# Kernel optimization log

Measured on AMD Instinct MI355X. Metric: run time of the kernel, lower is better.

Reference implementation:

```python
import jax, jax.numpy as jnp
import numpy as np
import math

NUM_HEADS = 8
FDIM = 64
NUM_BUCKETS = 32
MAX_DISTANCE = 128


def _relative_position_bucket(rel_pos, num_buckets=NUM_BUCKETS, max_distance=MAX_DISTANCE):
    nb = num_buckets // 2
    ret = (rel_pos >= 0).astype(jnp.int32) * nb
    n = jnp.abs(rel_pos)
    max_exact = nb // 2
    is_small = n < max_exact
    # safe log: clamp n to >=1 where large-branch is unused
    val_large = max_exact + (
        jnp.log(jnp.maximum(n, 1).astype(jnp.float32) / max_exact)
        / math.log(max_distance / max_exact) * (nb - max_exact)
    ).astype(jnp.int32)
    val_large = jnp.minimum(val_large, nb - 1)
    return ret + jnp.where(is_small, n, val_large)


def setup_inputs() -> dict:
    key = jax.random.key(0)
    k = jax.random.split(key, 5)
    B, Nin, F, T = 4, 64, FDIM, 1024
    N = NUM_HEADS * FDIM
    x = jax.random.normal(k[0], (B, Nin, F, T), dtype=jnp.float32)
    # kaiming_normal: std = 1/sqrt(fan_in)
    w_in = jax.random.normal(k[1], (NUM_HEADS, Nin), dtype=jnp.float32) / np.sqrt(Nin)
    w_qk = jax.random.normal(k[2], (2 * N, N), dtype=jnp.float32) / np.sqrt(N)
    w_out = jax.random.normal(k[3], (Nin, NUM_HEADS), dtype=jnp.float32) / np.sqrt(NUM_HEADS)
    rel_bias = jax.random.normal(k[4], (NUM_BUCKETS, NUM_HEADS), dtype=jnp.float32) * 0.02
    return {"x": x, "w_in": w_in, "w_qk": w_qk, "w_out": w_out, "rel_bias": rel_bias}


def reference(x, w_in, w_qk, w_out, rel_bias):
    B, Nin, F, T = x.shape
    h, f = NUM_HEADS, FDIM
    scale = f ** (-0.5)
    # proj_in: 1x1 conv2d Nin -> h
    xi = jnp.einsum('bcft,hc->bhft', x, w_in)          # [B,h,F,T]
    xr = xi.reshape(B, h * f, T)                        # b (h f) t
    v = xr.reshape(B, h, f, T).transpose(0, 1, 3, 2)    # [B,h,T,f]
    # qk: 1x1 conv1d N -> 2N
    qk = jnp.einsum('bct,dc->bdt', xr, w_qk)            # [B,2N,T]
    qk = qk.reshape(B, h, 2 * f, T).transpose(0, 1, 3, 2)  # [B,h,T,2f]
    q, k = qk[..., :f], qk[..., f:]
    sim = jnp.einsum('bhnd,bhmd->bhnm', q, k)           # [B,h,T,T]
    # relative position bias
    q_pos = jnp.arange(T)
    k_pos = jnp.arange(T)
    rel = k_pos[None, :] - q_pos[:, None]               # [T,T]
    buckets = _relative_position_bucket(rel)
    bias = rel_bias[buckets]                            # [T,T,h]
    bias = bias.transpose(2, 0, 1)[None]                # [1,h,T,T]
    sim = (sim + bias) * scale
    attn = jax.nn.softmax(sim, axis=-1)
    out = jnp.einsum('bhnm,bhmd->bhnd', attn, v)        # [B,h,T,f]
    out = out.transpose(0, 1, 3, 2)                     # [B,h,f,T]
    out = jnp.einsum('bhft,ch->bcft', out, w_out)       # [B,Nin,F,T]
    return out
```

## Files before the change

### kernel.cpp

```cpp
#include <hip/hip_runtime.h>
#include <math.h>

#define QSCALE 0.18033688011112042f

typedef __attribute__((ext_vector_type(4))) float  f32x4;
typedef __attribute__((ext_vector_type(2))) float  f32x2;
typedef __attribute__((ext_vector_type(8))) short  bf16x8;
typedef __attribute__((ext_vector_type(4))) short  bf16x4;
typedef __attribute__((ext_vector_type(4))) int    i32x4;

static __device__ __forceinline__ short f2bf(float f) {
    union { float f; unsigned u; } v; v.f = f;
    unsigned r = v.u + 0x7fffu + ((v.u >> 16) & 1u);
    return (short)(r >> 16);
}
static __device__ __forceinline__ int pk2bf(float a, float b) {
    return ((int)f2bf(a) & 0xffff) | ((int)f2bf(b) << 16);
}

#define MFMA16(A,B,C) __builtin_amdgcn_mfma_f32_16x16x32_bf16(A, B, C, 0, 0, 0)

__global__ void k_prep(const float* __restrict__ wqk, short* __restrict__ wqk_b) {
    int i = blockIdx.x * 256 + threadIdx.x;
    int D = i >> 9;
    float s = (D & 64) ? 1.0f : QSCALE;
    wqk_b[i] = f2bf(wqk[i] * s);
}

__global__ __launch_bounds__(256) void k_proj_in(
    const float* __restrict__ x, const float* __restrict__ w_in,
    short* __restrict__ xi_v, short* __restrict__ xr_t)
{
    __shared__ float w_s[512];
    __shared__ __align__(16) short tr[64 * 72];
    int tid = threadIdx.x;
    int tx = tid & 31, fy = tid >> 5;
    int tb = blockIdx.x, fb = blockIdx.y, b = blockIdx.z;
    w_s[tid] = w_in[tid & 511];
    w_s[(tid + 256) & 511] = w_in[(tid + 256) & 511];
    __syncthreads();

    int f = fb * 8 + fy;
    int t = tb * 64 + tx * 2;
    float acc[8][2];
    #pragma unroll
    for (int h = 0; h < 8; h++) { acc[h][0] = 0.f; acc[h][1] = 0.f; }

    const float* xp = x + ((size_t)b * 64 * 64 + (size_t)f) * 1024 + t;
    f32x2 buf[8];
    #pragma unroll
    for (int i = 0; i < 8; i++) buf[i] = *(const f32x2*)&xp[(size_t)i * 65536];
    #pragma unroll
    for (int c8 = 0; c8 < 64; c8 += 8) {
        f32x2 cur[8];
        #pragma unroll
        for (int i = 0; i < 8; i++) cur[i] = buf[i];
        if (c8 + 8 < 64) {
            #pragma unroll
            for (int i = 0; i < 8; i++)
                buf[i] = *(const f32x2*)&xp[(size_t)(c8 + 8 + i) * 65536];
        }
        #pragma unroll
        for (int i = 0; i < 8; i++)
            #pragma unroll
            for (int h = 0; h < 8; h++) {
                float wv = w_s[h * 64 + c8 + i];
                acc[h][0] = fmaf(cur[i][0], wv, acc[h][0]);
                acc[h][1] = fmaf(cur[i][1], wv, acc[h][1]);
            }
    }
    #pragma unroll
    for (int h = 0; h < 8; h++)
        *(int*)&xi_v[(((size_t)b * 8 + h) * 64 + f) * 1024 + t] = pk2bf(acc[h][0], acc[h][1]);
    #pragma unroll
    for (int h = 0; h < 8; h++) {
        tr[(tx * 2 + 0) * 72 + h * 8 + fy] = f2bf(acc[h][0]);
        tr[(tx * 2 + 1) * 72 + h * 8 + fy] = f2bf(acc[h][1]);
    }
    __syncthreads();
    int h2 = tid & 7, trow = tid >> 3;
    #pragma unroll
    for (int i = 0; i < 2; i++) {
        int t2 = trow + i * 32;
        i32x4 v = *(const i32x4*)&tr[t2 * 72 + h2 * 8];
        *(i32x4*)&xr_t[((size_t)b * 1024 + tb * 64 + t2) * 512 + h2 * 64 + fb * 8] = v;
    }
}

__global__ __launch_bounds__(256, 4) void k_qk(
    const short* __restrict__ wqk_b, const short* __restrict__ xr_t,
    short* __restrict__ qk_t)
{
    __shared__ __align__(16) short As[64 * 72];
    __shared__ __align__(16) short Bs[64 * 72];
    int tid = threadIdx.x;
    int w = tid >> 6, lane = tid & 63;
    int quad = lane >> 4, l16 = lane & 15;
    int t0 = blockIdx.x * 64;
    int Dt = blockIdx.y;
    int b  = blockIdx.z;

    f32x4 acc[4];
    #pragma unroll
    for (int tt = 0; tt < 4; tt++) acc[tt] = (f32x4){0.f,0.f,0.f,0.f};

    const short* Ag = wqk_b + (size_t)Dt * 64 * 512;
    const short* Bg = xr_t + ((size_t)b * 1024 + t0) * 512;

    int s_row = tid >> 2, s_col = (tid & 3) * 16;

    for (int kk = 0; kk < 512; kk += 64) {
        __syncthreads();
        #pragma unroll
        for (int i = 0; i < 2; i++) {
            *(i32x4*)&As[s_row * 72 + s_col + i * 8] =
                *(const i32x4*)&Ag[(size_t)s_row * 512 + kk + s_col + i * 8];
            *(i32x4*)&Bs[s_row * 72 + s_col + i * 8] =
                *(const i32x4*)&Bg[(size_t)s_row * 512 + kk + s_col + i * 8];
        }
        __syncthreads();
        bf16x8 af[2];
        #pragma unroll
        for (int kc = 0; kc < 2; kc++)
            af[kc] = *(const bf16x8*)&As[(w * 16 + l16) * 72 + kc * 32 + quad * 8];
        #pragma unroll
        for (int tt = 0; tt < 4; tt++) {
            bf16x8 bf0 = *(const bf16x8*)&Bs[(tt * 16 + l16) * 72 + quad * 8];
            bf16x8 bf1 = *(const bf16x8*)&Bs[(tt * 16 + l16) * 72 + 32 + quad * 8];
            acc[tt] = MFMA16(af[0], bf0, acc[tt]);
            acc[tt] = MFMA16(af[1], bf1, acc[tt]);
        }
    }
    int h = Dt >> 1;
    int d2 = (Dt & 1) * 64 + w * 16 + quad * 4;
    #pragma unroll
    for (int tt = 0; tt < 4; tt++) {
        bf16x4 pk;
        pk.x = f2bf(acc[tt][0]); pk.y = f2bf(acc[tt][1]);
        pk.z = f2bf(acc[tt][2]); pk.w = f2bf(acc[tt][3]);
        int t = t0 + tt * 16 + l16;
        *(bf16x4*)&qk_t[(((size_t)b * 8 + h) * 1024 + t) * 128 + d2] = pk;
    }
}

__global__ __launch_bounds__(256, 4) void k_attn(
    const short* __restrict__ qk_t, const short* __restrict__ xi_v,
    const float* __restrict__ rel_bias, float* __restrict__ o_part,
    float* __restrict__ lsum)
{
    __shared__ __align__(16) short Ks[64 * 72];
    __shared__ __align__(16) short Vs[64 * 72];
    __shared__ __align__(16) short Ps[4][16 * 72];
    __shared__ float elut[2048];
    int tid = threadIdx.x;
    int w = tid >> 6, lane = tid & 63;
    int quad = lane >> 4, l16 = lane & 15;
    int nb = blockIdx.x, bh = blockIdx.y, mh = blockIdx.z;
    int h = bh & 7;
    int n_base = nb * 64;

    for (int i = tid; i < 2047; i += 256) {
        int rel = i - 1023;
        int ret = (rel >= 0) ? 16 : 0;
        int na = rel < 0 ? -rel : rel;
        int idx;
        if (na < 8) idx = ret + na;
        else {
            int vl = 8 + (int)(log2f((float)na * 0.125f) * 2.0f);
            vl = vl > 15 ? 15 : vl;
            idx = ret + vl;
        }
        elut[i] = exp2f(rel_bias[idx * 8 + h] * QSCALE);
    }

    const short* qb = qk_t + (size_t)bh * (1024 * 128);
    const short* vb = xi_v + (size_t)bh * (64 * 1024);

    bf16x8 qf[2];
    #pragma unroll
    for (int kk = 0; kk < 2; kk++)
        qf[kk] = *(const bf16x8*)&qb[(size_t)(n_base + w * 16 + l16) * 128 + kk * 32 + quad * 8];

    f32x4 acc_o[4];
    #pragma unroll
    for (int dt = 0; dt < 4; dt++) acc_o[dt] = (f32x4){0.f,0.f,0.f,0.f};
    float l_st = 0.f;

    int srow = tid >> 2;
    int soff = (tid & 3) * 16;
    int m0 = mh * 512;
    i32x4 gk[2], gv[2];
    #pragma unroll
    for (int i = 0; i < 2; i++) {
        gk[i] = *(const i32x4*)&qb[(size_t)(m0 + srow) * 128 + 64 + soff + i * 8];
        gv[i] = *(const i32x4*)&vb[(size_t)srow * 1024 + m0 + soff + i * 8];
    }

    __syncthreads();

    #pragma unroll 1
    for (int it = 0; it < 8; it++) {
        *(i32x4*)&Ks[srow * 72 + soff]     = gk[0];
        *(i32x4*)&Ks[srow * 72 + soff + 8] = gk[1];
        *(i32x4*)&Vs[srow * 72 + soff]     = gv[0];
        *(i32x4*)&Vs[srow * 72 + soff + 8] = gv[1];
        __syncthreads();
        if (it < 7) {
            int m1 = m0 + 64;
            #pragma unroll
            for (int i = 0; i < 2; i++) {
                gk[i] = *(const i32x4*)&qb[(size_t)(m1 + srow) * 128 + 64 + soff + i * 8];
                gv[i] = *(const i32x4*)&vb[(size_t)srow * 1024 + m1 + soff + i * 8];
            }
        }

        f32x4 s[4];
        #pragma unroll
        for (int mt = 0; mt < 4; mt++) {
            bf16x8 kf0 = *(const bf16x8*)&Ks[(mt * 16 + l16) * 72 + quad * 8];
            bf16x8 kf1 = *(const bf16x8*)&Ks[(mt * 16 + l16) * 72 + 32 + quad * 8];
            f32x4 tacc = (f32x4){0.f,0.f,0.f,0.f};
            tacc = MFMA16(kf0, qf[0], tacc);
            tacc = MFMA16(kf1, qf[1], tacc);
            s[mt] = tacc;
        }

        int n = n_base + w * 16 + l16;
        #pragma unroll
        for (int mt = 0; mt < 4; mt++) {
            int rel0 = m0 + mt * 16 + quad * 4 - n + 1023;
            #pragma unroll
            for (int j = 0; j < 4; j++) {
                float p = exp2f(s[mt][j]) * elut[rel0 + j];
                s[mt][j] = p;
                l_st += p;
            }
        }
        #pragma unroll
        for (int mt = 0; mt < 4; mt++) {
            bf16x4 pk;
            pk.x = f2bf(s[mt][0]); pk.y = f2bf(s[mt][1]);
            pk.z = f2bf(s[mt][2]); pk.w = f2bf(s[mt][3]);
            *(bf16x4*)&Ps[w][l16 * 72 + mt * 16 + quad * 4] = pk;
        }
        #pragma unroll
        for (int si = 0; si < 2; si++) {
            bf16x8 pf = *(const bf16x8*)&Ps[w][l16 * 72 + si * 32 + quad * 8];
            #pragma unroll
            for (int dt = 0; dt < 4; dt++) {
                bf16x8 vf = *(const bf16x8*)&Vs[(dt * 16 + l16) * 72 + si * 32 + quad * 8];
                acc_o[dt] = MFMA16(pf, vf, acc_o[dt]);
            }
        }
        m0 += 64;
        __syncthreads();
    }
    #pragma unroll
    for (int dt = 0; dt < 4; dt++)
        *(f32x4*)&o_part[(((size_t)mh * 32 + bh) * 64 + dt * 16 + l16) * 1024 + n_base + w * 16 + quad * 4] = acc_o[dt];
    l_st += __shfl_xor(l_st, 16);
    l_st += __shfl_xor(l_st, 32);
    if (quad == 0)
        lsum[((size_t)bh * 2 + mh) * 1024 + n_base + w * 16 + l16] = l_st;
}

__global__ __launch_bounds__(512) void k_proj_out(
    const float* __restrict__ o_part, const float* __restrict__ lsum,
    const float* __restrict__ w_out, float* __restrict__ out)
{
    __shared__ float w_s[512];
    __shared__ float o_s[8][64];
    int tid = threadIdx.x;
    int tx = tid & 63, ty = tid >> 6;
    int tb = blockIdx.x, f = blockIdx.y, b = blockIdx.z;
    w_s[tid] = w_out[tid];
    int t = tb * 64 + tx;
    int bh = b * 8 + ty;
    float l0 = lsum[((size_t)bh * 2 + 0) * 1024 + t];
    float l1 = lsum[((size_t)bh * 2 + 1) * 1024 + t];
    float o0 = o_part[((size_t)(0 * 32 + bh) * 64 + f) * 1024 + t];
    float o1 = o_part[((size_t)(1 * 32 + bh) * 64 + f) * 1024 + t];
    o_s[ty][tx] = (o0 + o1) / (l0 + l1);
    __syncthreads();
    float ov[8];
    #pragma unroll
    for (int hh = 0; hh < 8; hh++) ov[hh] = o_s[hh][tx];
    #pragma unroll
    for (int j = 0; j < 8; j++) {
        int c = ty * 8 + j;
        float a = 0.f;
        #pragma unroll
        for (int hh = 0; hh < 8; hh++) a = fmaf(ov[hh], w_s[c * 8 + hh], a);
        out[(((size_t)b * 64 + c) * 64 + f) * 1024 + t] = a;
    }
}

extern "C" void kernel_launch(void* const* d_in, const int* in_sizes, int n_in,
                              void* d_out, int out_size, void* d_ws, size_t ws_size,
                              hipStream_t stream)
{
    const float* x        = (const float*)d_in[0];
    const float* w_in     = (const float*)d_in[1];
    const float* w_qk     = (const float*)d_in[2];
    const float* w_out    = (const float*)d_in[3];
    const float* rel_bias = (const float*)d_in[4];
    float* out = (float*)d_out;

    char* ws = (char*)d_ws;
    short* wqk_b  = (short*)(ws);
    short* xi_v   = (short*)(ws + (size_t)1  * (1 << 20));
    short* xr_t   = (short*)(ws + (size_t)5  * (1 << 20));
    short* qk_t   = (short*)(ws + (size_t)9  * (1 << 20));
    float* o_part = (float*)(ws + (size_t)17 * (1 << 20));
    float* lsum   = (float*)(ws + (size_t)33 * (1 << 20));

    hipLaunchKernelGGL(k_prep,     dim3(2048),       dim3(256), 0, stream, w_qk, wqk_b);
    hipLaunchKernelGGL(k_proj_in,  dim3(16, 8, 4),   dim3(256), 0, stream, x, w_in, xi_v, xr_t);
    hipLaunchKernelGGL(k_qk,       dim3(16, 16, 4),  dim3(256), 0, stream, wqk_b, xr_t, qk_t);
    hipLaunchKernelGGL(k_attn,     dim3(16, 32, 2),  dim3(256), 0, stream, qk_t, xi_v, rel_bias, o_part, lsum);
    hipLaunchKernelGGL(k_proj_out, dim3(16, 64, 4),  dim3(512), 0, stream, o_part, lsum, w_out, out);
}
```

Measured before the change: 163.5 us.

## Split attention key range across waves and reduce partial outputs in shared memory

The attention kernel now gives each wave a disjoint slice of keys for all 64 query rows, instead of a 16-row query slice over all keys. K and V fragments are loaded straight from global memory into registers, which removes the shared K/V staging and the per-iteration barriers. The bias LUT is shrunk to the 576 relative offsets this block actually touches and stored as rotated bf16 copies for aligned vector reads. Partial outputs from the four waves are summed through shared memory before one coalesced store. This trades more accumulator registers (occupancy hint lowered to 3), lower bias precision and a serialized cross-wave reduction for fewer LDS round-trips and syncs.

```diff
diff --git a/kernel.cpp b/kernel.cpp
--- a/kernel.cpp
+++ b/kernel.cpp
@@ -16,6 +16,10 @@
 }
 static __device__ __forceinline__ int pk2bf(float a, float b) {
     return ((int)f2bf(a) & 0xffff) | ((int)f2bf(b) << 16);
+}
+static __device__ __forceinline__ float bf2f(short s) {
+    union { unsigned u; float f; } v; v.u = ((unsigned)(unsigned short)s) << 16;
+    return v.f;
 }
 
 #define MFMA16(A,B,C) __builtin_amdgcn_mfma_f32_16x16x32_bf16(A, B, C, 0, 0, 0)
@@ -143,24 +147,26 @@
     }
 }
 
-__global__ __launch_bounds__(256, 4) void k_attn(
+__global__ __launch_bounds__(256, 3) void k_attn(
     const short* __restrict__ qk_t, const short* __restrict__ xi_v,
     const float* __restrict__ rel_bias, float* __restrict__ o_part,
     float* __restrict__ lsum)
 {
-    __shared__ __align__(16) short Ks[64 * 72];
-    __shared__ __align__(16) short Vs[64 * 72];
-    __shared__ __align__(16) short Ps[4][16 * 72];
-    __shared__ float elut[2048];
+    __shared__ __align__(16) short Ps[4][64 * 40];
+    __shared__ __align__(16) short lut_rot[4][144 * 4];
+    __shared__ __align__(16) float Or[64 * 68];
+    __shared__ float lsum_s[4][64];
+
     int tid = threadIdx.x;
     int w = tid >> 6, lane = tid & 63;
     int quad = lane >> 4, l16 = lane & 15;
     int nb = blockIdx.x, bh = blockIdx.y, mh = blockIdx.z;
     int h = bh & 7;
     int n_base = nb * 64;
-
-    for (int i = tid; i < 2047; i += 256) {
-        int rel = i - 1023;
+    int base_rel = mh * 512 - n_base - 63;
+
+    for (int i = tid; i < 576; i += 256) {
+        int rel = base_rel + i;
         int ret = (rel >= 0) ? 16 : 0;
         int na = rel < 0 ? -rel : rel;
         int idx;
@@ -170,98 +176,117 @@
             vl = vl > 15 ? 15 : vl;
             idx = ret + vl;
         }
-        elut[i] = exp2f(rel_bias[idx * 8 + h] * QSCALE);
-    }
+        Or[i] = exp2f(rel_bias[idx * 8 + h] * QSCALE);
+    }
+    __syncthreads();
+    for (int e = tid; e < 576; e += 256) {
+        int r = e / 144, k = e - r * 144;
+        int i0 = 4 * k + r;
+        bf16x4 pk;
+        pk.x = f2bf(Or[i0 > 575 ? 575 : i0]);
+        pk.y = f2bf(Or[i0 + 1 > 575 ? 575 : i0 + 1]);
+        pk.z = f2bf(Or[i0 + 2 > 575 ? 575 : i0 + 2]);
+        pk.w = f2bf(Or[i0 + 3 > 575 ? 575 : i0 + 3]);
+        *(bf16x4*)&lut_rot[r][k * 4] = pk;
+    }
+    __syncthreads();
 
     const short* qb = qk_t + (size_t)bh * (1024 * 128);
     const short* vb = xi_v + (size_t)bh * (64 * 1024);
 
-    bf16x8 qf[2];
-    #pragma unroll
-    for (int kk = 0; kk < 2; kk++)
-        qf[kk] = *(const bf16x8*)&qb[(size_t)(n_base + w * 16 + l16) * 128 + kk * 32 + quad * 8];
-
-    f32x4 acc_o[4];
-    #pragma unroll
-    for (int dt = 0; dt < 4; dt++) acc_o[dt] = (f32x4){0.f,0.f,0.f,0.f};
-    float l_st = 0.f;
-
-    int srow = tid >> 2;
-    int soff = (tid & 3) * 16;
-    int m0 = mh * 512;
-    i32x4 gk[2], gv[2];
-    #pragma unroll
-    for (int i = 0; i < 2; i++) {
-        gk[i] = *(const i32x4*)&qb[(size_t)(m0 + srow) * 128 + 64 + soff + i * 8];
-        gv[i] = *(const i32x4*)&vb[(size_t)srow * 1024 + m0 + soff + i * 8];
-    }
-
-    __syncthreads();
+    bf16x8 qf[4][2];
+    #pragma unroll
+    for (int nt = 0; nt < 4; nt++)
+        #pragma unroll
+        for (int kc = 0; kc < 2; kc++)
+            qf[nt][kc] = *(const bf16x8*)&qb[(size_t)(n_base + nt * 16 + l16) * 128 + kc * 32 + quad * 8];
+
+    f32x4 acc[4][4];
+    #pragma unroll
+    for (int nt = 0; nt < 4; nt++)
+        #pragma unroll
+        for (int dt = 0; dt < 4; dt++) acc[nt][dt] = (f32x4){0.f,0.f,0.f,0.f};
+    f32x4 lp = (f32x4){0.f,0.f,0.f,0.f};
+
+    short* psw = &Ps[w][0];
 
     #pragma unroll 1
-    for (int it = 0; it < 8; it++) {
-        *(i32x4*)&Ks[srow * 72 + soff]     = gk[0];
-        *(i32x4*)&Ks[srow * 72 + soff + 8] = gk[1];
-        *(i32x4*)&Vs[srow * 72 + soff]     = gv[0];
-        *(i32x4*)&Vs[srow * 72 + soff + 8] = gv[1];
+    for (int it = 0; it < 4; it++) {
+        int mloc  = it * 128 + w * 32;
+        int mbase = mh * 512 + mloc;
+        bf16x8 vf[4];
+        #pragma unroll
+        for (int dt = 0; dt < 4; dt++)
+            vf[dt] = *(const bf16x8*)&vb[(size_t)(dt * 16 + l16) * 1024 + mbase + quad * 8];
+
+        #pragma unroll
+        for (int mt = 0; mt < 2; mt++) {
+            bf16x8 kf0 = *(const bf16x8*)&qb[(size_t)(mbase + mt * 16 + l16) * 128 + 64 + quad * 8];
+            bf16x8 kf1 = *(const bf16x8*)&qb[(size_t)(mbase + mt * 16 + l16) * 128 + 96 + quad * 8];
+            #pragma unroll
+            for (int nt = 0; nt < 4; nt++) {
+                f32x4 s = (f32x4){0.f,0.f,0.f,0.f};
+                s = MFMA16(kf0, qf[nt][0], s);
+                s = MFMA16(kf1, qf[nt][1], s);
+                int rel0 = mloc + mt * 16 + quad * 4 - (nt * 16 + l16) + 63;
+                bf16x4 lv = *(const bf16x4*)&lut_rot[rel0 & 3][(rel0 >> 2) * 4];
+                f32x4 p;
+                p[0] = exp2f(s[0]) * bf2f(lv.x);
+                p[1] = exp2f(s[1]) * bf2f(lv.y);
+                p[2] = exp2f(s[2]) * bf2f(lv.z);
+                p[3] = exp2f(s[3]) * bf2f(lv.w);
+                lp[nt] += p[0] + p[1] + p[2] + p[3];
+                bf16x4 pk;
+                pk.x = f2bf(p[0]); pk.y = f2bf(p[1]);
+                pk.z = f2bf(p[2]); pk.w = f2bf(p[3]);
+                *(bf16x4*)&psw[(nt * 16 + l16) * 40 + mt * 16 + quad * 4] = pk;
+            }
+        }
+        #pragma unroll
+        for (int nt = 0; nt < 4; nt++) {
+            bf16x8 pf = *(const bf16x8*)&psw[(nt * 16 + l16) * 40 + quad * 8];
+            #pragma unroll
+            for (int dt = 0; dt < 4; dt++)
+                acc[nt][dt] = MFMA16(pf, vf[dt], acc[nt][dt]);
+        }
+    }
+
+    #pragma unroll
+    for (int nt = 0; nt < 4; nt++) {
+        float v = lp[nt];
+        v += __shfl_xor(v, 16);
+        v += __shfl_xor(v, 32);
+        if (quad == 0) lsum_s[w][nt * 16 + l16] = v;
+    }
+    __syncthreads();
+
+    #pragma unroll 1
+    for (int ww = 0; ww < 4; ww++) {
+        if (w == ww) {
+            #pragma unroll
+            for (int nt = 0; nt < 4; nt++)
+                #pragma unroll
+                for (int dt = 0; dt < 4; dt++) {
+                    float* dst = &Or[(dt * 16 + l16) * 68 + nt * 16 + quad * 4];
+                    if (ww == 0) *(f32x4*)dst = acc[nt][dt];
+                    else {
+                        f32x4 old = *(const f32x4*)dst;
+                        *(f32x4*)dst = old + acc[nt][dt];
+                    }
+                }
+        }
         __syncthreads();
-        if (it < 7) {
-            int m1 = m0 + 64;
-            #pragma unroll
-            for (int i = 0; i < 2; i++) {
-                gk[i] = *(const i32x4*)&qb[(size_t)(m1 + srow) * 128 + 64 + soff + i * 8];
-                gv[i] = *(const i32x4*)&vb[(size_t)srow * 1024 + m1 + soff + i * 8];
-            }
-        }
-
-        f32x4 s[4];
-        #pragma unroll
-        for (int mt = 0; mt < 4; mt++) {
-            bf16x8 kf0 = *(const bf16x8*)&Ks[(mt * 16 + l16) * 72 + quad * 8];
-            bf16x8 kf1 = *(const bf16x8*)&Ks[(mt * 16 + l16) * 72 + 32 + quad * 8];
-            f32x4 tacc = (f32x4){0.f,0.f,0.f,0.f};
-            tacc = MFMA16(kf0, qf[0], tacc);
-            tacc = MFMA16(kf1, qf[1], tacc);
-            s[mt] = tacc;
-        }
-
-        int n = n_base + w * 16 + l16;
-        #pragma unroll
-        for (int mt = 0; mt < 4; mt++) {
-            int rel0 = m0 + mt * 16 + quad * 4 - n + 1023;
-            #pragma unroll
-            for (int j = 0; j < 4; j++) {
-                float p = exp2f(s[mt][j]) * elut[rel0 + j];
-                s[mt][j] = p;
-                l_st += p;
-            }
-        }
-        #pragma unroll
-        for (int mt = 0; mt < 4; mt++) {
-            bf16x4 pk;
-            pk.x = f2bf(s[mt][0]); pk.y = f2bf(s[mt][1]);
-            pk.z = f2bf(s[mt][2]); pk.w = f2bf(s[mt][3]);
-            *(bf16x4*)&Ps[w][l16 * 72 + mt * 16 + quad * 4] = pk;
-        }
-        #pragma unroll
-        for (int si = 0; si < 2; si++) {
-            bf16x8 pf = *(const bf16x8*)&Ps[w][l16 * 72 + si * 32 + quad * 8];
-            #pragma unroll
-            for (int dt = 0; dt < 4; dt++) {
-                bf16x8 vf = *(const bf16x8*)&Vs[(dt * 16 + l16) * 72 + si * 32 + quad * 8];
-                acc_o[dt] = MFMA16(pf, vf, acc_o[dt]);
-            }
-        }
-        m0 += 64;
-        __syncthreads();
-    }
-    #pragma unroll
-    for (int dt = 0; dt < 4; dt++)
-        *(f32x4*)&o_part[(((size_t)mh * 32 + bh) * 64 + dt * 16 + l16) * 1024 + n_base + w * 16 + quad * 4] = acc_o[dt];
-    l_st += __shfl_xor(l_st, 16);
-    l_st += __shfl_xor(l_st, 32);
-    if (quad == 0)
-        lsum[((size_t)bh * 2 + mh) * 1024 + n_base + w * 16 + l16] = l_st;
+    }
+
+    int d = tid >> 2, n0 = (tid & 3) * 16;
+    float* op = &o_part[(((size_t)mh * 32 + bh) * 64 + d) * 1024 + n_base + n0];
+    #pragma unroll
+    for (int i = 0; i < 4; i++)
+        *(f32x4*)&op[i * 4] = *(const f32x4*)&Or[d * 68 + n0 + i * 4];
+    if (tid < 64) {
+        float s = lsum_s[0][tid] + lsum_s[1][tid] + lsum_s[2][tid] + lsum_s[3][tid];
+        lsum[((size_t)bh * 2 + mh) * 1024 + n_base + tid] = s;
+    }
 }
 
 __global__ __launch_bounds__(512) void k_proj_out(
```

New measurement: 191.9 us. 1.17x slower.
